# Kernel tuning notes

Measured on AMD Instinct MI355X. Metric: run time of the kernel, lower is better.

Reference implementation:

```python
import jax, jax.numpy as jnp
import numpy as np

B, NQ, N, D_IN, D_KEY, D_MODEL = 8, 2048, 2048, 512, 512, 512


def setup_inputs() -> dict:
    key = jax.random.key(0)
    k1, k2, k3, k4, k5, k6 = jax.random.split(key, 6)
    lim_k = np.sqrt(6.0 / (D_IN + D_KEY))
    lim_v = np.sqrt(6.0 / (D_IN + D_MODEL))
    return {
        "node_features": jax.random.normal(k1, (B, N, D_IN), dtype=jnp.float32),
        "query": jax.random.normal(k2, (B, NQ, D_IN), dtype=jnp.float32),
        "mask": jax.random.bernoulli(k3, 0.3, (NQ, B, N)),  # True = masked out
        "wq": jax.random.uniform(k4, (D_IN, D_KEY), jnp.float32, -lim_k, lim_k),
        "wk": jax.random.uniform(k5, (D_IN, D_KEY), jnp.float32, -lim_k, lim_k),
        "wv": jax.random.uniform(k6, (D_IN, D_MODEL), jnp.float32, -lim_v, lim_v),
    }


def reference(node_features, query, mask, wq, wk, wv):
    # Projections
    Q = query @ wq              # [B, NQ, d_key]
    K = node_features @ wk      # [B, N, d_key]
    V = node_features @ wv      # [B, N, d_model]
    # Raw scores [B, NQ, N]
    scores = jnp.einsum("bqd,bnd->bqn", Q, K)
    b, nq, n = scores.shape
    # Faithful to tf: reshape to (NQ, B, N), mask with float32.min, reshape back
    s = scores.reshape(nq, b, n)
    masked = jnp.where(mask, jnp.finfo(jnp.float32).min, s).reshape(b, nq, n)
    # Scale AFTER masking (as in the original), then softmax over keys
    attn = jax.nn.softmax(masked / jnp.sqrt(jnp.float32(K.shape[-1])), axis=-1)
    return attn @ V             # [B, NQ, d_model]
```

## Files before the change

### kernel.cpp

```cpp
#include <hip/hip_runtime.h>

typedef __attribute__((ext_vector_type(8))) short bf16x8;
typedef __attribute__((ext_vector_type(4))) float f32x4;

__device__ __forceinline__ unsigned short f2bf(float f) {
  unsigned int u = __builtin_bit_cast(unsigned int, f);
  u += 0x7fffu + ((u >> 16) & 1u);
  return (unsigned short)(u >> 16);
}

#define GLD16(gp, lp) __builtin_amdgcn_global_load_lds( \
    (const __attribute__((address_space(1))) unsigned int*)(gp), \
    (__attribute__((address_space(3))) unsigned int*)(lp), 16, 0, 0)

__global__ __launch_bounds__(256) void pack_mask(
    const unsigned char* __restrict__ m, unsigned long long* __restrict__ pm)
{
  __shared__ int mode1;
  if (threadIdx.x == 0) mode1 = 0;
  __syncthreads();

  const int g = blockIdx.x * 256 + threadIdx.x;
  const size_t base = (size_t)g * 64;

  uint4 v[4];
  const uint4* p1 = (const uint4*)(m + base);
  v[0] = p1[0]; v[1] = p1[1]; v[2] = p1[2]; v[3] = p1[3];
  unsigned int probe = 0;
#pragma unroll
  for (int j = 0; j < 4; ++j)
    probe |= (v[j].x | v[j].y | v[j].z | v[j].w);
  if (probe & 0x0000ff00u) mode1 = 1;
  __syncthreads();

  unsigned long long bits = 0;
  if (mode1) {
#pragma unroll
    for (int j = 0; j < 4; ++j) {
      unsigned int w[4] = {v[j].x, v[j].y, v[j].z, v[j].w};
#pragma unroll
      for (int q = 0; q < 4; ++q) {
        unsigned int u = w[q];
#pragma unroll
        for (int b = 0; b < 4; ++b)
          if ((u >> (8 * b)) & 0xffu) bits |= 1ull << (j * 16 + q * 4 + b);
      }
    }
  } else {
    const uint4* p4 = (const uint4*)(m + base * 4);
#pragma unroll
    for (int j = 0; j < 16; ++j) {
      uint4 w = p4[j];
      if (w.x) bits |= 1ull << (j * 4 + 0);
      if (w.y) bits |= 1ull << (j * 4 + 1);
      if (w.z) bits |= 1ull << (j * 4 + 2);
      if (w.w) bits |= 1ull << (j * 4 + 3);
    }
  }
  pm[g] = bits;
}

__global__ void prep(const float* __restrict__ query, const float* __restrict__ node,
                     const float* __restrict__ wq, const float* __restrict__ wk,
                     const float* __restrict__ wv,
                     unsigned short* __restrict__ Xq, unsigned short* __restrict__ Xn,
                     unsigned short* __restrict__ oq, unsigned short* __restrict__ ok,
                     unsigned short* __restrict__ ov, float* __restrict__ sums)
{
  const int b = blockIdx.x;
  if (b < 16384) {
    int i = b * 256 + threadIdx.x;
    const float* src;
    unsigned short* dst;
    int j;
    if (i < 2097152) { src = query; dst = Xq; j = i; }
    else             { src = node;  dst = Xn; j = i - 2097152; }
    float4 v = ((const float4*)src)[j];
    ushort4 o;
    o.x = f2bf(v.x); o.y = f2bf(v.y); o.z = f2bf(v.z); o.w = f2bf(v.w);
    ((ushort4*)dst)[j] = o;
  } else if (b < 19456) {
    int idx = (b - 16384) * 256 + threadIdx.x;
    int w = idx >> 18;
    int rem = idx & 262143;
    int n = rem >> 9, k = rem & 511;
    const float* W = (w == 0) ? wq : (w == 1) ? wk : wv;
    unsigned short* O = (w == 0) ? oq : (w == 1) ? ok : ov;
    O[n * 512 + k] = f2bf(W[k * 512 + n]);
  } else {
    int idx = (b - 19456) * 256 + threadIdx.x;
    sums[idx] = 0.0f;
  }
}

__device__ __forceinline__ void core128(
    const unsigned short* __restrict__ Ab, const unsigned short* __restrict__ Bb,
    void* __restrict__ Cb, long ldA, long ldB, long ldO, int nk,
    long bm, long bn, char* smem, int mode, const float* __restrict__ sums_ro)
{
  const int tid = threadIdx.x;
  const int lane = tid & 63;
  const int wid = tid >> 6;
  const int wr = wid >> 1, wc = wid & 1;
  const int fr = lane & 15, fq = lane >> 4;

  const int srow = tid >> 2;
  const int sch = (tid & 3) ^ ((srow >> 1) & 3);

  char* bufs[4] = { smem, smem + 16384, smem + 32768, smem + 49152 };

#define STAGE_C(buf, kt) do { \
    const long k0_ = (long)(kt) << 5; \
    GLD16(Ab + (bm + srow) * ldA + k0_ + sch * 8,        (buf) + tid * 16); \
    GLD16(Ab + (bm + 64 + srow) * ldA + k0_ + sch * 8,   (buf) + 4096 + tid * 16); \
    GLD16(Bb + (bn + srow) * ldB + k0_ + sch * 8,        (buf) + 8192 + tid * 16); \
    GLD16(Bb + (bn + 64 + srow) * ldB + k0_ + sch * 8,   (buf) + 12288 + tid * 16); \
  } while (0)

  int aoff[4], boff[4];
#pragma unroll
  for (int i = 0; i < 4; ++i) {
    const int ra = wr * 64 + i * 16 + fr;
    aoff[i] = ra * 64 + (fq ^ ((ra >> 1) & 3)) * 16;
    const int rb = wc * 64 + i * 16 + fr;
    boff[i] = 8192 + rb * 64 + (fq ^ ((rb >> 1) & 3)) * 16;
  }

  f32x4 acc[4][4] = {};

  STAGE_C(bufs[0], 0);
  STAGE_C(bufs[1], 1);
  STAGE_C(bufs[2], 2);
  char* c0 = bufs[0]; char* c1 = bufs[1]; char* c2 = bufs[2]; char* c3 = bufs[3];

  for (int t = 0; t < nk; ++t) {
    __builtin_amdgcn_sched_barrier(0);
    __builtin_amdgcn_s_barrier();
    if (t + 3 < nk) {
      STAGE_C(c3, t + 3);
      asm volatile("s_waitcnt vmcnt(12)" ::: "memory");
    } else if (t + 3 == nk) {
      asm volatile("s_waitcnt vmcnt(8)" ::: "memory");
    } else if (t + 2 == nk) {
      asm volatile("s_waitcnt vmcnt(4)" ::: "memory");
    } else {
      asm volatile("s_waitcnt vmcnt(0)" ::: "memory");
    }
    __builtin_amdgcn_s_barrier();
    __builtin_amdgcn_sched_barrier(0);

    bf16x8 a[4];
#pragma unroll
    for (int mi = 0; mi < 4; ++mi)
      a[mi] = *(const bf16x8*)(c0 + aoff[mi]);
    __builtin_amdgcn_s_setprio(1);
#pragma unroll
    for (int nj = 0; nj < 4; ++nj) {
      const bf16x8 b = *(const bf16x8*)(c0 + boff[nj]);
#pragma unroll
      for (int mi = 0; mi < 4; ++mi)
        acc[mi][nj] = __builtin_amdgcn_mfma_f32_16x16x32_bf16(a[mi], b, acc[mi][nj], 0, 0, 0);
    }
    __builtin_amdgcn_s_setprio(0);

    char* tmp = c0; c0 = c1; c1 = c2; c2 = c3; c3 = tmp;
  }
#undef STAGE_C

  if (mode == 0) {
    unsigned short* C = (unsigned short*)Cb;
#pragma unroll
    for (int mi = 0; mi < 4; ++mi)
#pragma unroll
      for (int nj = 0; nj < 4; ++nj) {
        const long row = bm + wr * 64 + mi * 16 + fq * 4;
        const long col = bn + wc * 64 + nj * 16 + fr;
#pragma unroll
        for (int r = 0; r < 4; ++r)
          C[(row + r) * ldO + col] = f2bf(acc[mi][nj][r]);
      }
  } else {
    float* C = (float*)Cb;
#pragma unroll
    for (int mi = 0; mi < 4; ++mi) {
      const long rowb = bm + wr * 64 + mi * 16 + fq * 4;
#pragma unroll
      for (int r = 0; r < 4; ++r) {
        const long row = rowb + r;
        const float iv = 1.0f / sums_ro[row];
        const long colb = bn + wc * 64 + fr;
#pragma unroll
        for (int nj = 0; nj < 4; ++nj)
          C[row * ldO + colb + nj * 16] = acc[mi][nj][r] * iv;
      }
    }
  }
}

__global__ __launch_bounds__(256, 2) void gemm_scores(
    const unsigned short* __restrict__ Qg, const unsigned short* __restrict__ Kg,
    unsigned short* __restrict__ Eg, const unsigned long long* __restrict__ pm,
    float* __restrict__ sums)
{
  extern __shared__ char smem[];
  const long z = blockIdx.x;
  const long bm = (long)blockIdx.y * 128;
  const long bn = (long)blockIdx.z * 256;

  const unsigned short* Ab = Qg + z * 1048576;
  const unsigned short* Bb = Kg + z * 1048576;
  unsigned short* C = Eg + z * 4194304;
  const unsigned long long* pmask = pm + z * 65536;
  float* sumz = sums + z * 2048;

  const int tid = threadIdx.x;
  const int lane = tid & 63;
  const int wid = tid >> 6;
  const int wr = wid >> 1, wc = wid & 1;
  const int fr = lane & 15, fq = lane >> 4;

  const int srow = tid >> 2;
  const int sch = (tid & 3) ^ ((srow >> 1) & 3);

  char* bufs[3] = { smem, smem + 24576, smem + 49152 };

#define STAGE_S(buf, kt) do { \
    const long k0_ = (long)(kt) << 5; \
    GLD16(Ab + (bm + srow) * 512 + k0_ + sch * 8,        (buf) + tid * 16); \
    GLD16(Ab + (bm + 64 + srow) * 512 + k0_ + sch * 8,   (buf) + 4096 + tid * 16); \
    GLD16(Bb + (bn + srow) * 512 + k0_ + sch * 8,        (buf) + 8192 + tid * 16); \
    GLD16(Bb + (bn + 64 + srow) * 512 + k0_ + sch * 8,   (buf) + 12288 + tid * 16); \
    GLD16(Bb + (bn + 128 + srow) * 512 + k0_ + sch * 8,  (buf) + 16384 + tid * 16); \
    GLD16(Bb + (bn + 192 + srow) * 512 + k0_ + sch * 8,  (buf) + 20480 + tid * 16); \
  } while (0)

  int aoff[4], boff[8];
#pragma unroll
  for (int i = 0; i < 4; ++i) {
    const int r = wr * 64 + i * 16 + fr;
    aoff[i] = r * 64 + (fq ^ ((r >> 1) & 3)) * 16;
  }
#pragma unroll
  for (int i = 0; i < 8; ++i) {
    const int r = wc * 128 + i * 16 + fr;
    boff[i] = 8192 + r * 64 + (fq ^ ((r >> 1) & 3)) * 16;
  }

  f32x4 acc[4][8] = {};

  STAGE_S(bufs[0], 0);
  STAGE_S(bufs[1], 1);
  char* c0 = bufs[0]; char* c1 = bufs[1]; char* c2 = bufs[2];

  const int nk = 16;
  for (int t = 0; t < nk; ++t) {
    __builtin_amdgcn_sched_barrier(0);
    __builtin_amdgcn_s_barrier();
    if (t + 2 < nk) {
      STAGE_S(c2, t + 2);
      asm volatile("s_waitcnt vmcnt(12)" ::: "memory");
    } else if (t + 2 == nk) {
      asm volatile("s_waitcnt vmcnt(6)" ::: "memory");
    } else {
      asm volatile("s_waitcnt vmcnt(0)" ::: "memory");
    }
    __builtin_amdgcn_s_barrier();
    __builtin_amdgcn_sched_barrier(0);

    bf16x8 a[4];
#pragma unroll
    for (int mi = 0; mi < 4; ++mi)
      a[mi] = *(const bf16x8*)(c0 + aoff[mi]);
    __builtin_amdgcn_s_setprio(1);
#pragma unroll
    for (int nj = 0; nj < 8; ++nj) {
      const bf16x8 b = *(const bf16x8*)(c0 + boff[nj]);
#pragma unroll
      for (int mi = 0; mi < 4; ++mi)
        acc[mi][nj] = __builtin_amdgcn_mfma_f32_16x16x32_bf16(a[mi], b, acc[mi][nj], 0, 0, 0);
    }
    __builtin_amdgcn_s_setprio(0);

    char* tmp = c0; c0 = c1; c1 = c2; c2 = tmp;
  }
#undef STAGE_S

  const float SCALE = 0.04419417382415922f;
  const long wbase = (bn >> 6) + wc * 2;
#pragma unroll
  for (int mi = 0; mi < 4; ++mi) {
    const long rowb = bm + wr * 64 + mi * 16 + fq * 4;
#pragma unroll
    for (int r = 0; r < 4; ++r) {
      const long row = rowb + r;
      const unsigned long long w0 = pmask[row * 32 + wbase];
      const unsigned long long w1 = pmask[row * 32 + wbase + 1];
      unsigned short* Crow = C + row * 2048 + bn + wc * 128 + fr;
      float s = 0.f;
#pragma unroll
      for (int ni = 0; ni < 8; ++ni) {
        const unsigned long long w = (ni < 4) ? w0 : w1;
        const int sh = (ni & 3) * 16 + fr;
        float e = ((w >> sh) & 1ull) ? 0.0f : __expf(acc[mi][ni][r] * SCALE);
        s += e;
        Crow[ni * 16] = f2bf(e);
      }
      s += __shfl_xor(s, 1); s += __shfl_xor(s, 2);
      s += __shfl_xor(s, 4); s += __shfl_xor(s, 8);
      if (fr == 0) atomicAdd(&sumz[row], s);
    }
  }
}

__global__ __launch_bounds__(256, 2) void gemm_proj(
    const unsigned short* __restrict__ Xq, const unsigned short* __restrict__ Xn,
    const unsigned short* __restrict__ Wqt, const unsigned short* __restrict__ Wkt,
    const unsigned short* __restrict__ Wvt,
    unsigned short* __restrict__ Q, unsigned short* __restrict__ Kb,
    unsigned short* __restrict__ Vt)
{
  extern __shared__ char smem[];
  const int z = blockIdx.z;
  if (z == 0) {
    core128(Xq, Wqt, Q, 512, 512, 512, 16,
            (long)blockIdx.x * 128, (long)blockIdx.y * 128, smem, 0, nullptr);
  } else if (z == 1) {
    core128(Xn, Wkt, Kb, 512, 512, 512, 16,
            (long)blockIdx.x * 128, (long)blockIdx.y * 128, smem, 0, nullptr);
  } else {
    core128(Wvt, Xn, Vt, 512, 512, 16384, 16,
            (long)blockIdx.y * 128, (long)blockIdx.x * 128, smem, 0, nullptr);
  }
}

__global__ __launch_bounds__(256, 2) void gemm_pv(
    const unsigned short* __restrict__ E, const unsigned short* __restrict__ Vt,
    const float* __restrict__ sums, float* __restrict__ O)
{
  extern __shared__ char smem[];
  const long z = blockIdx.x;
  core128(E + z * 4194304, Vt + z * 2048, O + z * 1048576,
          2048, 16384, 512, 64,
          (long)blockIdx.y * 128, (long)blockIdx.z * 128, smem,
          2, sums + z * 2048);
}

extern "C" void kernel_launch(void* const* d_in, const int* in_sizes, int n_in,
                              void* d_out, int out_size, void* d_ws, size_t ws_size,
                              hipStream_t stream) {
  const float* node  = (const float*)d_in[0];
  const float* query = (const float*)d_in[1];
  const unsigned char* mask = (const unsigned char*)d_in[2];
  const float* wq = (const float*)d_in[3];
  const float* wk = (const float*)d_in[4];
  const float* wv = (const float*)d_in[5];
  float* out = (float*)d_out;

  char* ws = (char*)d_ws;
  unsigned short* Q   = (unsigned short*)(ws);
  unsigned short* Kb  = (unsigned short*)(ws + 16777216);
  unsigned short* Vt  = (unsigned short*)(ws + 33554432);
  unsigned short* E   = (unsigned short*)(ws + 50331648);
  unsigned short* Xq  = (unsigned short*)(ws + 50331648);
  unsigned short* Xn  = (unsigned short*)(ws + 50331648 + 16777216);
  unsigned short* Wqt = (unsigned short*)(ws + 50331648 + 33554432);
  unsigned short* Wkt = Wqt + 262144;
  unsigned short* Wvt = Wkt + 262144;
  float* sums = (float*)(ws + 117440512);
  unsigned long long* pm = (unsigned long long*)(ws + 118489088);

  pack_mask<<<2048, 256, 0, stream>>>(mask, pm);
  prep<<<19520, 256, 0, stream>>>(query, node, wq, wk, wv,
                                  Xq, Xn, Wqt, Wkt, Wvt, sums);

  dim3 gp(128, 4, 3);
  gemm_proj<<<gp, 256, 65536, stream>>>(Xq, Xn, Wqt, Wkt, Wvt, Q, Kb, Vt);

  dim3 gs(8, 16, 8);
  gemm_scores<<<gs, 256, 73728, stream>>>(Q, Kb, E, pm, sums);

  dim3 gv(8, 16, 4);
  gemm_pv<<<gv, 256, 65536, stream>>>(E, Vt, sums, out);
}
```

Baseline: 198.9 us.

## Unify GEMMs on 128x128 triple-buffered core to raise occupancy to three blocks

Replaces the dedicated 128x256 scores kernel with the shared 128x128 core, adding a mode that does mask, exp, bf16 store and row-sum atomics in its epilogue. The shared core drops from four LDS stages to three (48KB), so all three GEMMs can declare three blocks per CU. The PV grid is also reordered so consecutive blocks walk the output-column tiles. The aim is more resident waves to hide latency, at the cost of a shallower prefetch pipeline and smaller score tiles that reload Q more often and issue more atomics.

```diff
diff --git a/kernel.cpp b/kernel.cpp
--- a/kernel.cpp
+++ b/kernel.cpp
@@ -96,7 +96,9 @@
 __device__ __forceinline__ void core128(
     const unsigned short* __restrict__ Ab, const unsigned short* __restrict__ Bb,
     void* __restrict__ Cb, long ldA, long ldB, long ldO, int nk,
-    long bm, long bn, char* smem, int mode, const float* __restrict__ sums_ro)
+    long bm, long bn, char* smem, int mode,
+    const unsigned long long* __restrict__ pmask, float* __restrict__ sumz,
+    const float* __restrict__ sums_ro)
 {
   const int tid = threadIdx.x;
   const int lane = tid & 63;
@@ -107,7 +109,7 @@
   const int srow = tid >> 2;
   const int sch = (tid & 3) ^ ((srow >> 1) & 3);
 
-  char* bufs[4] = { smem, smem + 16384, smem + 32768, smem + 49152 };
+  char* bufs[3] = { smem, smem + 16384, smem + 32768 };
 
 #define STAGE_C(buf, kt) do { \
     const long k0_ = (long)(kt) << 5; \
@@ -130,16 +132,13 @@
 
   STAGE_C(bufs[0], 0);
   STAGE_C(bufs[1], 1);
-  STAGE_C(bufs[2], 2);
-  char* c0 = bufs[0]; char* c1 = bufs[1]; char* c2 = bufs[2]; char* c3 = bufs[3];
+  char* c0 = bufs[0]; char* c1 = bufs[1]; char* c2 = bufs[2];
 
   for (int t = 0; t < nk; ++t) {
     __builtin_amdgcn_sched_barrier(0);
     __builtin_amdgcn_s_barrier();
-    if (t + 3 < nk) {
-      STAGE_C(c3, t + 3);
-      asm volatile("s_waitcnt vmcnt(12)" ::: "memory");
-    } else if (t + 3 == nk) {
+    if (t + 2 < nk) {
+      STAGE_C(c2, t + 2);
       asm volatile("s_waitcnt vmcnt(8)" ::: "memory");
     } else if (t + 2 == nk) {
       asm volatile("s_waitcnt vmcnt(4)" ::: "memory");
@@ -163,10 +162,11 @@
     }
     __builtin_amdgcn_s_setprio(0);
 
-    char* tmp = c0; c0 = c1; c1 = c2; c2 = c3; c3 = tmp;
+    char* tmp = c0; c0 = c1; c1 = c2; c2 = tmp;
   }
 #undef STAGE_C
 
+  const float SCALE = 0.04419417382415922f;
   if (mode == 0) {
     unsigned short* C = (unsigned short*)Cb;
 #pragma unroll
@@ -179,6 +179,30 @@
         for (int r = 0; r < 4; ++r)
           C[(row + r) * ldO + col] = f2bf(acc[mi][nj][r]);
       }
+  } else if (mode == 1) {
+    unsigned short* C = (unsigned short*)Cb;
+    const long wword = (bn >> 6) + wc;
+#pragma unroll
+    for (int mi = 0; mi < 4; ++mi) {
+      const long rowb = bm + wr * 64 + mi * 16 + fq * 4;
+#pragma unroll
+      for (int r = 0; r < 4; ++r) {
+        const long row = rowb + r;
+        const unsigned long long w = pmask[row * 32 + wword];
+        unsigned short* Crow = C + row * ldO + bn + wc * 64 + fr;
+        float s = 0.f;
+#pragma unroll
+        for (int nj = 0; nj < 4; ++nj) {
+          const int sh = nj * 16 + fr;
+          float e = ((w >> sh) & 1ull) ? 0.0f : __expf(acc[mi][nj][r] * SCALE);
+          s += e;
+          Crow[nj * 16] = f2bf(e);
+        }
+        s += __shfl_xor(s, 1); s += __shfl_xor(s, 2);
+        s += __shfl_xor(s, 4); s += __shfl_xor(s, 8);
+        if (fr == 0) atomicAdd(&sumz[row], s);
+      }
+    }
   } else {
     float* C = (float*)Cb;
 #pragma unroll
@@ -197,122 +221,7 @@
   }
 }
 
-__global__ __launch_bounds__(256, 2) void gemm_scores(
-    const unsigned short* __restrict__ Qg, const unsigned short* __restrict__ Kg,
-    unsigned short* __restrict__ Eg, const unsigned long long* __restrict__ pm,
-    float* __restrict__ sums)
-{
-  extern __shared__ char smem[];
-  const long z = blockIdx.x;
-  const long bm = (long)blockIdx.y * 128;
-  const long bn = (long)blockIdx.z * 256;
-
-  const unsigned short* Ab = Qg + z * 1048576;
-  const unsigned short* Bb = Kg + z * 1048576;
-  unsigned short* C = Eg + z * 4194304;
-  const unsigned long long* pmask = pm + z * 65536;
-  float* sumz = sums + z * 2048;
-
-  const int tid = threadIdx.x;
-  const int lane = tid & 63;
-  const int wid = tid >> 6;
-  const int wr = wid >> 1, wc = wid & 1;
-  const int fr = lane & 15, fq = lane >> 4;
-
-  const int srow = tid >> 2;
-  const int sch = (tid & 3) ^ ((srow >> 1) & 3);
-
-  char* bufs[3] = { smem, smem + 24576, smem + 49152 };
-
-#define STAGE_S(buf, kt) do { \
-    const long k0_ = (long)(kt) << 5; \
-    GLD16(Ab + (bm + srow) * 512 + k0_ + sch * 8,        (buf) + tid * 16); \
-    GLD16(Ab + (bm + 64 + srow) * 512 + k0_ + sch * 8,   (buf) + 4096 + tid * 16); \
-    GLD16(Bb + (bn + srow) * 512 + k0_ + sch * 8,        (buf) + 8192 + tid * 16); \
-    GLD16(Bb + (bn + 64 + srow) * 512 + k0_ + sch * 8,   (buf) + 12288 + tid * 16); \
-    GLD16(Bb + (bn + 128 + srow) * 512 + k0_ + sch * 8,  (buf) + 16384 + tid * 16); \
-    GLD16(Bb + (bn + 192 + srow) * 512 + k0_ + sch * 8,  (buf) + 20480 + tid * 16); \
-  } while (0)
-
-  int aoff[4], boff[8];
-#pragma unroll
-  for (int i = 0; i < 4; ++i) {
-    const int r = wr * 64 + i * 16 + fr;
-    aoff[i] = r * 64 + (fq ^ ((r >> 1) & 3)) * 16;
-  }
-#pragma unroll
-  for (int i = 0; i < 8; ++i) {
-    const int r = wc * 128 + i * 16 + fr;
-    boff[i] = 8192 + r * 64 + (fq ^ ((r >> 1) & 3)) * 16;
-  }
-
-  f32x4 acc[4][8] = {};
-
-  STAGE_S(bufs[0], 0);
-  STAGE_S(bufs[1], 1);
-  char* c0 = bufs[0]; char* c1 = bufs[1]; char* c2 = bufs[2];
-
-  const int nk = 16;
-  for (int t = 0; t < nk; ++t) {
-    __builtin_amdgcn_sched_barrier(0);
-    __builtin_amdgcn_s_barrier();
-    if (t + 2 < nk) {
-      STAGE_S(c2, t + 2);
-      asm volatile("s_waitcnt vmcnt(12)" ::: "memory");
-    } else if (t + 2 == nk) {
-      asm volatile("s_waitcnt vmcnt(6)" ::: "memory");
-    } else {
-      asm volatile("s_waitcnt vmcnt(0)" ::: "memory");
-    }
-    __builtin_amdgcn_s_barrier();
-    __builtin_amdgcn_sched_barrier(0);
-
-    bf16x8 a[4];
-#pragma unroll
-    for (int mi = 0; mi < 4; ++mi)
-      a[mi] = *(const bf16x8*)(c0 + aoff[mi]);
-    __builtin_amdgcn_s_setprio(1);
-#pragma unroll
-    for (int nj = 0; nj < 8; ++nj) {
-      const bf16x8 b = *(const bf16x8*)(c0 + boff[nj]);
-#pragma unroll
-      for (int mi = 0; mi < 4; ++mi)
-        acc[mi][nj] = __builtin_amdgcn_mfma_f32_16x16x32_bf16(a[mi], b, acc[mi][nj], 0, 0, 0);
-    }
-    __builtin_amdgcn_s_setprio(0);
-
-    char* tmp = c0; c0 = c1; c1 = c2; c2 = tmp;
-  }
-#undef STAGE_S
-
-  const float SCALE = 0.04419417382415922f;
-  const long wbase = (bn >> 6) + wc * 2;
-#pragma unroll
-  for (int mi = 0; mi < 4; ++mi) {
-    const long rowb = bm + wr * 64 + mi * 16 + fq * 4;
-#pragma unroll
-    for (int r = 0; r < 4; ++r) {
-      const long row = rowb + r;
-      const unsigned long long w0 = pmask[row * 32 + wbase];
-      const unsigned long long w1 = pmask[row * 32 + wbase + 1];
-      unsigned short* Crow = C + row * 2048 + bn + wc * 128 + fr;
-      float s = 0.f;
-#pragma unroll
-      for (int ni = 0; ni < 8; ++ni) {
-        const unsigned long long w = (ni < 4) ? w0 : w1;
-        const int sh = (ni & 3) * 16 + fr;
-        float e = ((w >> sh) & 1ull) ? 0.0f : __expf(acc[mi][ni][r] * SCALE);
-        s += e;
-        Crow[ni * 16] = f2bf(e);
-      }
-      s += __shfl_xor(s, 1); s += __shfl_xor(s, 2);
-      s += __shfl_xor(s, 4); s += __shfl_xor(s, 8);
-      if (fr == 0) atomicAdd(&sumz[row], s);
-    }
-  }
-}
-
-__global__ __launch_bounds__(256, 2) void gemm_proj(
+__global__ __launch_bounds__(256, 3) void gemm_proj(
     const unsigned short* __restrict__ Xq, const unsigned short* __restrict__ Xn,
     const unsigned short* __restrict__ Wqt, const unsigned short* __restrict__ Wkt,
     const unsigned short* __restrict__ Wvt,
@@ -323,17 +232,33 @@
   const int z = blockIdx.z;
   if (z == 0) {
     core128(Xq, Wqt, Q, 512, 512, 512, 16,
-            (long)blockIdx.x * 128, (long)blockIdx.y * 128, smem, 0, nullptr);
+            (long)blockIdx.x * 128, (long)blockIdx.y * 128, smem, 0,
+            nullptr, nullptr, nullptr);
   } else if (z == 1) {
     core128(Xn, Wkt, Kb, 512, 512, 512, 16,
-            (long)blockIdx.x * 128, (long)blockIdx.y * 128, smem, 0, nullptr);
+            (long)blockIdx.x * 128, (long)blockIdx.y * 128, smem, 0,
+            nullptr, nullptr, nullptr);
   } else {
     core128(Wvt, Xn, Vt, 512, 512, 16384, 16,
-            (long)blockIdx.y * 128, (long)blockIdx.x * 128, smem, 0, nullptr);
-  }
-}
-
-__global__ __launch_bounds__(256, 2) void gemm_pv(
+            (long)blockIdx.y * 128, (long)blockIdx.x * 128, smem, 0,
+            nullptr, nullptr, nullptr);
+  }
+}
+
+__global__ __launch_bounds__(256, 3) void gemm_scores(
+    const unsigned short* __restrict__ Qg, const unsigned short* __restrict__ Kg,
+    unsigned short* __restrict__ Eg, const unsigned long long* __restrict__ pm,
+    float* __restrict__ sums)
+{
+  extern __shared__ char smem[];
+  const long z = blockIdx.x;
+  core128(Qg + z * 1048576, Kg + z * 1048576, Eg + z * 4194304,
+          512, 512, 2048, 16,
+          (long)blockIdx.y * 128, (long)blockIdx.z * 128, smem, 1,
+          pm + z * 65536, sums + z * 2048, nullptr);
+}
+
+__global__ __launch_bounds__(256, 3) void gemm_pv(
     const unsigned short* __restrict__ E, const unsigned short* __restrict__ Vt,
     const float* __restrict__ sums, float* __restrict__ O)
 {
@@ -341,8 +266,8 @@
   const long z = blockIdx.x;
   core128(E + z * 4194304, Vt + z * 2048, O + z * 1048576,
           2048, 16384, 512, 64,
-          (long)blockIdx.y * 128, (long)blockIdx.z * 128, smem,
-          2, sums + z * 2048);
+          (long)blockIdx.z * 128, (long)blockIdx.y * 128, smem, 2,
+          nullptr, nullptr, sums + z * 2048);
 }
 
 extern "C" void kernel_launch(void* const* d_in, const int* in_sizes, int n_in,
@@ -374,11 +299,11 @@
                                   Xq, Xn, Wqt, Wkt, Wvt, sums);
 
   dim3 gp(128, 4, 3);
-  gemm_proj<<<gp, 256, 65536, stream>>>(Xq, Xn, Wqt, Wkt, Wvt, Q, Kb, Vt);
-
-  dim3 gs(8, 16, 8);
-  gemm_scores<<<gs, 256, 73728, stream>>>(Q, Kb, E, pm, sums);
-
-  dim3 gv(8, 16, 4);
-  gemm_pv<<<gv, 256, 65536, stream>>>(E, Vt, sums, out);
-}
+  gemm_proj<<<gp, 256, 49152, stream>>>(Xq, Xn, Wqt, Wkt, Wvt, Q, Kb, Vt);
+
+  dim3 gs(8, 16, 16);
+  gemm_scores<<<gs, 256, 49152, stream>>>(Q, Kb, E, pm, sums);
+
+  dim3 gv(8, 4, 16);
+  gemm_pv<<<gv, 256, 49152, stream>>>(E, Vt, sums, out);
+}
```

Measured after the change: 205.1 us. +3.1%, slower.
